# Optimization experiments

Hardware: AMD Instinct MI355X
Metric: run time of the kernel (lower is better)

The kernel has to match this reference:

```python
import jax, jax.numpy as jnp
import numpy as np

D_MODEL = 1024
D_STATE = 16
D_CONV = 4
EXPAND = 2
D_INNER = D_MODEL * EXPAND
B_SZ = 2
SEQ = 4096


def setup_inputs() -> dict:
    key = jax.random.key(0)
    ks = jax.random.split(key, 11)
    rn = lambda i, shape, scale=1.0: jax.random.normal(ks[i], shape, jnp.float32) * scale
    return {
        "x": rn(0, (B_SZ, SEQ, D_MODEL)),
        "W_in": rn(1, (D_MODEL, D_INNER), D_MODEL ** -0.5),
        "b_in": rn(2, (D_INNER,), 0.01),
        "conv_w": rn(3, (D_INNER, 1, D_CONV), 0.1),   # torch depthwise layout [out_ch, in_ch/groups=1, k]
        "conv_b": rn(4, (D_INNER,), 0.01),
        # A scaled so tanh(A) is contractive -> stable recurrence over 4096 steps
        "A": rn(5, (D_STATE, D_STATE), 0.1),
        "Bp": rn(6, (D_STATE,)),   # B parameter [d_state, 1] flattened
        "Cp": rn(7, (D_STATE,)),   # C parameter [1, d_state] flattened
        "Dp": rn(8, (1,)),
        "W_out": rn(9, (D_INNER, D_MODEL), D_INNER ** -0.5),
        "b_out": rn(10, (D_MODEL,), 0.01),
    }


def reference(x, W_in, b_in, conv_w, conv_b, A, Bp, Cp, Dp, W_out, b_out):
    Bsz, S, _ = x.shape
    d_inner = W_in.shape[1]
    # input projection
    u = x @ W_in + b_in                              # [B, S, d_inner]
    # causal depthwise conv (torch pads k-1 both sides then slices [:S])
    u = u.transpose(0, 2, 1)                         # [B, d_inner, S]
    u = jax.lax.conv_general_dilated(
        u, conv_w, window_strides=(1,), padding=[(D_CONV - 1, 0)],
        dimension_numbers=("NCH", "OIH", "NCH"),
        feature_group_count=d_inner) + conv_b[None, :, None]
    u = u.transpose(0, 2, 1)                         # [B, S, d_inner]
    # per-channel scalar SSM shared across channels: h_t = tanh(A) h_{t-1} + B u_t; y_t = C h_t + D u_t
    At = jnp.tanh(A)                                 # [ds, ds]
    def step(h, u_t):                                # h: [B, d_inner, ds], u_t: [B, d_inner]
        h = jnp.einsum("ij,bdj->bdi", At, h) + u_t[..., None] * Bp
        y = jnp.einsum("j,bdj->bd", Cp, h) + Dp[0] * u_t
        return h, y
    h0 = jnp.zeros((Bsz, d_inner, Bp.shape[0]), x.dtype)
    _, ys = jax.lax.scan(step, h0, u.transpose(1, 0, 2))  # ys: [S, B, d_inner]
    y = jax.nn.silu(ys.transpose(1, 0, 2))           # [B, S, d_inner]
    return y @ W_out + b_out                         # [B, S, d_model]
```

## Files before the change

kernel.cpp:

```cpp
#include <hip/hip_runtime.h>

typedef unsigned short u16;
typedef float  f32x4  __attribute__((ext_vector_type(4)));
typedef __bf16 bf16x8 __attribute__((ext_vector_type(8)));
typedef u16    u16x2  __attribute__((ext_vector_type(2)));
typedef u16    u16x4  __attribute__((ext_vector_type(4)));

#define D_MODEL 1024
#define D_INNER 2048
#define B_SZ    2
#define SEQ     4096
#define MROWS   (B_SZ * SEQ)
#define LTAPS   64
#define VROW    136

__device__ __forceinline__ u16 f2bf(float f) {
    return __builtin_bit_cast(u16, (__bf16)f);
}
__device__ __forceinline__ float bf2f(u16 h) {
    unsigned u = ((unsigned)h) << 16;
    return __builtin_bit_cast(float, u);
}

typedef __attribute__((address_space(1))) void gv_t;
typedef __attribute__((address_space(3))) void lv_t;
__device__ __forceinline__ void glds16(const u16* g, u16* l) {
    __builtin_amdgcn_global_load_lds((gv_t*)g, (lv_t*)l, 16, 0, 0);
}
#define WAIT_VM0   0x0F70
#define WAIT_LGKM0 0xC07F

__device__ __forceinline__ void transpose_tile(
    const float* __restrict__ in, u16* __restrict__ out,
    int R, int C, int c0, int r0, int tid, float (*tile)[33])
{
    const int tx = tid & 31, ty = tid >> 5;
    for (int k = 0; k < 32; k += 8)
        tile[ty + k][tx] = in[(size_t)(r0 + ty + k) * C + c0 + tx];
    __syncthreads();
    for (int k = 0; k < 32; k += 8)
        out[(size_t)(c0 + ty + k) * R + r0 + tx] = f2bf(tile[tx][ty + k]);
}

__global__ __launch_bounds__(256) void prep_kernel(
    const float* __restrict__ x, u16* __restrict__ xb,
    const float* __restrict__ Win, u16* __restrict__ WinT,
    const float* __restrict__ Wout, u16* __restrict__ WoutT,
    const float* __restrict__ A, const float* __restrict__ Bp,
    const float* __restrict__ Cp, const float* __restrict__ Dp,
    u16* __restrict__ Amat64)
{
    __shared__ float tile[32][33];
    __shared__ float fs[LTAPS];
    const int bx = blockIdx.x, tid = threadIdx.x;
    if (bx < 8192) {
        size_t i = ((size_t)bx * 256 + tid) * 4;
        f32x4 v = *(const f32x4*)(x + i);
        u16x4 o;
        o.x = f2bf(v.x); o.y = f2bf(v.y); o.z = f2bf(v.z); o.w = f2bf(v.w);
        *(u16x4*)(xb + i) = o;
    } else if (bx < 10240) {
        const int flat = bx - 8192;
        transpose_tile(Win, WinT, 1024, 2048,
                       (flat & 63) * 32, (flat >> 6) * 32, tid, tile);
    } else if (bx < 12288) {
        const int flat = bx - 10240;
        transpose_tile(Wout, WoutT, 2048, 1024,
                       (flat & 31) * 32, (flat >> 5) * 32, tid, tile);
    } else {
        if (tid < 64) {
            const int i = tid & 15;
            float Atr[16];
            for (int j = 0; j < 16; j++) Atr[j] = tanhf(A[i * 16 + j]);
            float p = Bp[i];
            const float c  = Cp[i];
            const float d0 = Dp[0];
            for (int t = 0; t < LTAPS; t++) {
                float fv = c * p;
                fv += __shfl_xor(fv, 1); fv += __shfl_xor(fv, 2);
                fv += __shfl_xor(fv, 4); fv += __shfl_xor(fv, 8);
                if (tid == 0) fs[t] = fv + (t == 0 ? d0 : 0.f);
                float n0 = 0.f, n1 = 0.f, n2 = 0.f, n3 = 0.f;
                #pragma unroll
                for (int j = 0; j < 4; j++) {
                    n0 = fmaf(Atr[j],      __shfl(p, j),      n0);
                    n1 = fmaf(Atr[j + 4],  __shfl(p, j + 4),  n1);
                    n2 = fmaf(Atr[j + 8],  __shfl(p, j + 8),  n2);
                    n3 = fmaf(Atr[j + 12], __shfl(p, j + 12), n3);
                }
                p = (n0 + n1) + (n2 + n3);
            }
        }
        __syncthreads();
        for (int idx = tid; idx < 64 * 128; idx += 256) {
            const int i = idx >> 7, j = idx & 127;
            const int tau = 64 + i - j;
            float v = (tau >= 0 && tau < LTAPS) ? fs[tau] : 0.f;
            Amat64[idx] = f2bf(v);
        }
    }
}

template <int MODE>
__global__ __launch_bounds__(256) void gemm_bt_kernel(
    const u16* __restrict__ A, const u16* __restrict__ BT,
    void* __restrict__ Cout, const float* __restrict__ bias,
    int M, int N, int K)
{
    __shared__ u16 As[128 * 32];
    __shared__ u16 Bs[128 * 32];
    const int tid = threadIdx.x, lane = tid & 63, wid = tid >> 6;
    const int nTiles = gridDim.x;
    const int bid = blockIdx.x + nTiles * blockIdx.y;
    const int xcd = bid & 7;
    const int loc = bid >> 3;
    const int mt  = xcd * (gridDim.y >> 3) + (loc & 7);
    const int nt  = loc >> 3;
    const int m0 = mt * 128, n0 = nt * 128;
    const int sr = wid * 32 + (lane >> 2);
    const int sc = (lane & 3) * 8;
    const u16* ga = A  + (size_t)(m0 + sr) * K + sc;
    const u16* gb = BT + (size_t)(n0 + sr) * K + sc;
    u16* la = As + wid * 1024;
    u16* lb = Bs + wid * 1024;
    const int wm = (wid & 1) * 64, wn = (wid >> 1) * 64;
    const int fr = lane & 15, fq = lane >> 4;
    f32x4 acc[4][4] = {};
    glds16(ga, la);
    glds16(ga + (size_t)16 * K, la + 512);
    glds16(gb, lb);
    glds16(gb + (size_t)16 * K, lb + 512);
    const int iters = K >> 5;
    for (int it = 0; it < iters; ++it) {
        __builtin_amdgcn_s_waitcnt(WAIT_VM0);
        __builtin_amdgcn_s_barrier();
        bf16x8 af[4], bfr[4];
        #pragma unroll
        for (int i = 0; i < 4; i++)
            af[i]  = *(const bf16x8*)(As + (wm + i * 16 + fr) * 32 + fq * 8);
        #pragma unroll
        for (int i = 0; i < 4; i++)
            bfr[i] = *(const bf16x8*)(Bs + (wn + i * 16 + fr) * 32 + fq * 8);
        asm volatile("" ::: "memory");
        __builtin_amdgcn_s_waitcnt(WAIT_LGKM0);
        __builtin_amdgcn_s_barrier();
        if (it + 1 < iters) {
            const int k0 = (it + 1) << 5;
            glds16(ga + k0, la);
            glds16(ga + k0 + (size_t)16 * K, la + 512);
            glds16(gb + k0, lb);
            glds16(gb + k0 + (size_t)16 * K, lb + 512);
        }
        #pragma unroll
        for (int mi = 0; mi < 4; mi++)
            #pragma unroll
            for (int ni = 0; ni < 4; ni++)
                acc[mi][ni] = __builtin_amdgcn_mfma_f32_16x16x32_bf16(
                    bfr[ni], af[mi], acc[mi][ni], 0, 0, 0);
    }
    for (int ni = 0; ni < 4; ni++) {
        const int colb = n0 + wn + ni * 16 + fq * 4;
        const f32x4 bv = *(const f32x4*)(bias + colb);
        for (int mi = 0; mi < 4; mi++) {
            const int row = m0 + wm + mi * 16 + fr;
            f32x4 v = acc[mi][ni];
            v.x += bv.x; v.y += bv.y; v.z += bv.z; v.w += bv.w;
            if constexpr (MODE == 0) {
                u16x4 o;
                o.x = f2bf(v.x); o.y = f2bf(v.y); o.z = f2bf(v.z); o.w = f2bf(v.w);
                *(u16x4*)((u16*)Cout + (size_t)row * N + colb) = o;
            } else {
                *(f32x4*)((float*)Cout + (size_t)row * N + colb) = v;
            }
        }
    }
}

__global__ __launch_bounds__(256) void conv_fir_mfma_kernel(
    const u16* __restrict__ u, const float* __restrict__ cw,
    const float* __restrict__ cb, const u16* __restrict__ Amat64,
    u16* __restrict__ Y)
{
    __shared__ u16 VT[128 * VROW];
    const int tid = threadIdx.x;
    const int c0 = blockIdx.x * 128, t0 = blockIdx.y * 64, b = blockIdx.z;
    {
        const int tx = tid & 63, ty = tid >> 6;
        const int cg = c0 + tx * 2;
        const f32x4 wA = *(const f32x4*)(cw + cg * 4);
        const f32x4 wB = *(const f32x4*)(cw + cg * 4 + 4);
        const float cb0 = cb[cg], cb1 = cb[cg + 1];
        const u16* ucol = u + (size_t)b * SEQ * D_INNER + cg;
        const int s0 = t0 - 64 + ty * 32;
        u16* vr0 = VT + (tx * 2)     * VROW + ty * 32;
        u16* vr1 = VT + (tx * 2 + 1) * VROW + ty * 32;
        if (t0 == 0 && ty < 2) {
            const u16x4 z = {0, 0, 0, 0};
            #pragma unroll
            for (int j = 0; j < 8; j++) {
                *(u16x4*)(vr0 + j * 4) = z;
                *(u16x4*)(vr1 + j * 4) = z;
            }
        } else {
            float am3 = 0.f, am2 = 0.f, am1 = 0.f;
            float bm3 = 0.f, bm2 = 0.f, bm1 = 0.f;
            if (s0 > 0) {
                u16x2 d3 = *(const u16x2*)(ucol + (size_t)(s0 - 3) * D_INNER);
                u16x2 d2 = *(const u16x2*)(ucol + (size_t)(s0 - 2) * D_INNER);
                u16x2 d1 = *(const u16x2*)(ucol + (size_t)(s0 - 1) * D_INNER);
                am3 = bf2f(d3.x); bm3 = bf2f(d3.y);
                am2 = bf2f(d2.x); bm2 = bf2f(d2.y);
                am1 = bf2f(d1.x); bm1 = bf2f(d1.y);
            }
            #pragma unroll 2
            for (int j = 0; j < 8; j++) {
                const u16* p = ucol + (size_t)(s0 + j * 4) * D_INNER;
                u16x2 r0 = *(const u16x2*)(p);
                u16x2 r1 = *(const u16x2*)(p + (size_t)D_INNER);
                u16x2 r2 = *(const u16x2*)(p + (size_t)2 * D_INNER);
                u16x2 r3 = *(const u16x2*)(p + (size_t)3 * D_INNER);
                float a0 = bf2f(r0.x), b0 = bf2f(r0.y);
                float a1 = bf2f(r1.x), b1 = bf2f(r1.y);
                float a2 = bf2f(r2.x), b2 = bf2f(r2.y);
                float a3 = bf2f(r3.x), b3 = bf2f(r3.y);
                u16x4 oa, ob;
                oa.x = f2bf(cb0 + wA.x * am3 + wA.y * am2 + wA.z * am1 + wA.w * a0);
                oa.y = f2bf(cb0 + wA.x * am2 + wA.y * am1 + wA.z * a0  + wA.w * a1);
                oa.z = f2bf(cb0 + wA.x * am1 + wA.y * a0  + wA.z * a1  + wA.w * a2);
                oa.w = f2bf(cb0 + wA.x * a0  + wA.y * a1  + wA.z * a2  + wA.w * a3);
                ob.x = f2bf(cb1 + wB.x * bm3 + wB.y * bm2 + wB.z * bm1 + wB.w * b0);
                ob.y = f2bf(cb1 + wB.x * bm2 + wB.y * bm1 + wB.z * b0  + wB.w * b1);
                ob.z = f2bf(cb1 + wB.x * bm1 + wB.y * b0  + wB.z * b1  + wB.w * b2);
                ob.w = f2bf(cb1 + wB.x * b0  + wB.y * b1  + wB.z * b2  + wB.w * b3);
                *(u16x4*)(vr0 + j * 4) = oa;
                *(u16x4*)(vr1 + j * 4) = ob;
                am3 = a1; am2 = a2; am1 = a3;
                bm3 = b1; bm2 = b2; bm1 = b3;
            }
        }
    }
    __syncthreads();
    const int lane = tid & 63, wid = tid >> 6;
    const int wm = (wid & 1) * 32, wn = (wid >> 1) * 64;
    const int fr = lane & 15, fq = lane >> 4;
    f32x4 acc[2][4] = {};
    #pragma unroll
    for (int kq = 0; kq < 4; kq++) {
        const int k0 = kq * 32;
        bf16x8 af[2], bfr[4];
        #pragma unroll
        for (int mi = 0; mi < 2; mi++)
            af[mi] = *(const bf16x8*)(Amat64 + (wm + mi * 16 + fr) * 128 + k0 + fq * 8);
        #pragma unroll
        for (int ni = 0; ni < 4; ni++)
            bfr[ni] = *(const bf16x8*)(VT + (wn + ni * 16 + fr) * VROW + k0 + fq * 8);
        #pragma unroll
        for (int mi = 0; mi < 2; mi++)
            #pragma unroll
            for (int ni = 0; ni < 4; ni++)
                acc[mi][ni] = __builtin_amdgcn_mfma_f32_16x16x32_bf16(
                    bfr[ni], af[mi], acc[mi][ni], 0, 0, 0);
    }
    #pragma unroll
    for (int ni = 0; ni < 4; ni++) {
        const int cbase = c0 + wn + ni * 16 + fq * 4;
        #pragma unroll
        for (int mi = 0; mi < 2; mi++) {
            const int trow = t0 + wm + mi * 16 + fr;
            f32x4 v = acc[mi][ni];
            u16x4 o;
            o.x = f2bf(v.x / (1.f + __expf(-v.x)));
            o.y = f2bf(v.y / (1.f + __expf(-v.y)));
            o.z = f2bf(v.z / (1.f + __expf(-v.z)));
            o.w = f2bf(v.w / (1.f + __expf(-v.w)));
            *(u16x4*)(Y + ((size_t)(b * SEQ + trow)) * D_INNER + cbase) = o;
        }
    }
}

extern "C" void kernel_launch(void* const* d_in, const int* in_sizes, int n_in,
                              void* d_out, int out_size, void* d_ws, size_t ws_size,
                              hipStream_t stream)
{
    const float* x    = (const float*)d_in[0];
    const float* Win  = (const float*)d_in[1];
    const float* bin  = (const float*)d_in[2];
    const float* cw   = (const float*)d_in[3];
    const float* cb   = (const float*)d_in[4];
    const float* A    = (const float*)d_in[5];
    const float* Bp   = (const float*)d_in[6];
    const float* Cp   = (const float*)d_in[7];
    const float* Dp   = (const float*)d_in[8];
    const float* Wout = (const float*)d_in[9];
    const float* bout = (const float*)d_in[10];
    float* out = (float*)d_out;

    char* ws = (char*)d_ws;
    u16* xb     = (u16*)(ws);
    u16* WinT   = (u16*)(ws + 16777216);
    u16* WoutT  = (u16*)(ws + 20971520);
    u16* u      = (u16*)(ws + 25165824);
    u16* Y      = (u16*)(ws + 58720256);
    u16* Amat64 = (u16*)(ws + 92274688);

    prep_kernel<<<12289, 256, 0, stream>>>(x, xb, Win, WinT, Wout, WoutT,
                                           A, Bp, Cp, Dp, Amat64);
    gemm_bt_kernel<0><<<dim3(16, 64), 256, 0, stream>>>(xb, WinT, u, bin,
                                                        MROWS, D_INNER, D_MODEL);
    conv_fir_mfma_kernel<<<dim3(16, 64, 2), 256, 0, stream>>>(u, cw, cb, Amat64, Y);
    gemm_bt_kernel<1><<<dim3(8, 64), 256, 0, stream>>>(Y, WoutT, out, bout,
                                                       MROWS, D_MODEL, D_INNER);
}
```

Measured before the change: 241.1 us.

## Double-buffer GEMM LDS tiles and enlarge FIR conv time tile to 128

```diff
diff --git a/kernel.cpp b/kernel.cpp
--- a/kernel.cpp
+++ b/kernel.cpp
@@ -12,7 +12,8 @@
 #define SEQ     4096
 #define MROWS   (B_SZ * SEQ)
 #define LTAPS   64
-#define VROW    136
+#define KFIR    192
+#define CVROW   200
 
 __device__ __forceinline__ u16 f2bf(float f) {
     return __builtin_bit_cast(u16, (__bf16)f);
@@ -28,7 +29,9 @@
     __builtin_amdgcn_global_load_lds((gv_t*)g, (lv_t*)l, 16, 0, 0);
 }
 #define WAIT_VM0   0x0F70
+#define WAIT_VM4   0x0F74
 #define WAIT_LGKM0 0xC07F
+#define SCHED_FENCE() asm volatile("" ::: "memory")
 
 __device__ __forceinline__ void transpose_tile(
     const float* __restrict__ in, u16* __restrict__ out,
@@ -48,7 +51,7 @@
     const float* __restrict__ Wout, u16* __restrict__ WoutT,
     const float* __restrict__ A, const float* __restrict__ Bp,
     const float* __restrict__ Cp, const float* __restrict__ Dp,
-    u16* __restrict__ Amat64)
+    u16* __restrict__ Amat192)
 {
     __shared__ float tile[32][33];
     __shared__ float fs[LTAPS];
@@ -92,11 +95,11 @@
             }
         }
         __syncthreads();
-        for (int idx = tid; idx < 64 * 128; idx += 256) {
-            const int i = idx >> 7, j = idx & 127;
+        for (int idx = tid; idx < 128 * KFIR; idx += 256) {
+            const int i = idx / KFIR, j = idx % KFIR;
             const int tau = 64 + i - j;
             float v = (tau >= 0 && tau < LTAPS) ? fs[tau] : 0.f;
-            Amat64[idx] = f2bf(v);
+            Amat192[idx] = f2bf(v);
         }
     }
 }
@@ -107,8 +110,8 @@
     void* __restrict__ Cout, const float* __restrict__ bias,
     int M, int N, int K)
 {
-    __shared__ u16 As[128 * 32];
-    __shared__ u16 Bs[128 * 32];
+    __shared__ u16 As[2][128 * 32];
+    __shared__ u16 Bs[2][128 * 32];
     const int tid = threadIdx.x, lane = tid & 63, wid = tid >> 6;
     const int nTiles = gridDim.x;
     const int bid = blockIdx.x + nTiles * blockIdx.y;
@@ -121,34 +124,44 @@
     const int sc = (lane & 3) * 8;
     const u16* ga = A  + (size_t)(m0 + sr) * K + sc;
     const u16* gb = BT + (size_t)(n0 + sr) * K + sc;
-    u16* la = As + wid * 1024;
-    u16* lb = Bs + wid * 1024;
+    const int lo = wid * 1024;
     const int wm = (wid & 1) * 64, wn = (wid >> 1) * 64;
     const int fr = lane & 15, fq = lane >> 4;
     f32x4 acc[4][4] = {};
-    glds16(ga, la);
-    glds16(ga + (size_t)16 * K, la + 512);
-    glds16(gb, lb);
-    glds16(gb + (size_t)16 * K, lb + 512);
+    glds16(ga,                    As[0] + lo);
+    glds16(ga + (size_t)16 * K,   As[0] + lo + 512);
+    glds16(gb,                    Bs[0] + lo);
+    glds16(gb + (size_t)16 * K,   Bs[0] + lo + 512);
+    glds16(ga + 32,               As[1] + lo);
+    glds16(ga + 32 + (size_t)16 * K, As[1] + lo + 512);
+    glds16(gb + 32,               Bs[1] + lo);
+    glds16(gb + 32 + (size_t)16 * K, Bs[1] + lo + 512);
     const int iters = K >> 5;
     for (int it = 0; it < iters; ++it) {
-        __builtin_amdgcn_s_waitcnt(WAIT_VM0);
+        if (it + 1 < iters) __builtin_amdgcn_s_waitcnt(WAIT_VM4);
+        else                __builtin_amdgcn_s_waitcnt(WAIT_VM0);
         __builtin_amdgcn_s_barrier();
+        SCHED_FENCE();
+        const u16* Ab = As[it & 1];
+        const u16* Bb = Bs[it & 1];
         bf16x8 af[4], bfr[4];
         #pragma unroll
         for (int i = 0; i < 4; i++)
-            af[i]  = *(const bf16x8*)(As + (wm + i * 16 + fr) * 32 + fq * 8);
+            af[i]  = *(const bf16x8*)(Ab + (wm + i * 16 + fr) * 32 + fq * 8);
         #pragma unroll
         for (int i = 0; i < 4; i++)
-            bfr[i] = *(const bf16x8*)(Bs + (wn + i * 16 + fr) * 32 + fq * 8);
-        asm volatile("" ::: "memory");
+            bfr[i] = *(const bf16x8*)(Bb + (wn + i * 16 + fr) * 32 + fq * 8);
+        SCHED_FENCE();
         __builtin_amdgcn_s_waitcnt(WAIT_LGKM0);
         __builtin_amdgcn_s_barrier();
-        if (it + 1 < iters) {
-            const int k0 = (it + 1) << 5;
-            glds16(ga + k0, la);
+        SCHED_FENCE();
+        if (it + 2 < iters) {
+            const int k0 = (it + 2) << 5;
+            u16* la = As[it & 1] + lo;
+            u16* lb = Bs[it & 1] + lo;
+            glds16(ga + k0,                  la);
             glds16(ga + k0 + (size_t)16 * K, la + 512);
-            glds16(gb + k0, lb);
+            glds16(gb + k0,                  lb);
             glds16(gb + k0 + (size_t)16 * K, lb + 512);
         }
         #pragma unroll
@@ -178,12 +191,12 @@
 
 __global__ __launch_bounds__(256) void conv_fir_mfma_kernel(
     const u16* __restrict__ u, const float* __restrict__ cw,
-    const float* __restrict__ cb, const u16* __restrict__ Amat64,
+    const float* __restrict__ cb, const u16* __restrict__ Amat192,
     u16* __restrict__ Y)
 {
-    __shared__ u16 VT[128 * VROW];
+    __shared__ u16 VT[128 * CVROW];
     const int tid = threadIdx.x;
-    const int c0 = blockIdx.x * 128, t0 = blockIdx.y * 64, b = blockIdx.z;
+    const int c0 = blockIdx.x * 128, t0 = blockIdx.y * 128, b = blockIdx.z;
     {
         const int tx = tid & 63, ty = tid >> 6;
         const int cg = c0 + tx * 2;
@@ -191,30 +204,28 @@
         const f32x4 wB = *(const f32x4*)(cw + cg * 4 + 4);
         const float cb0 = cb[cg], cb1 = cb[cg + 1];
         const u16* ucol = u + (size_t)b * SEQ * D_INNER + cg;
-        const int s0 = t0 - 64 + ty * 32;
-        u16* vr0 = VT + (tx * 2)     * VROW + ty * 32;
-        u16* vr1 = VT + (tx * 2 + 1) * VROW + ty * 32;
-        if (t0 == 0 && ty < 2) {
-            const u16x4 z = {0, 0, 0, 0};
-            #pragma unroll
-            for (int j = 0; j < 8; j++) {
+        const int sbase = t0 - 64 + ty * 48;
+        u16* vr0 = VT + (tx * 2)     * CVROW + ty * 48;
+        u16* vr1 = VT + (tx * 2 + 1) * CVROW + ty * 48;
+        float am3 = 0.f, am2 = 0.f, am1 = 0.f;
+        float bm3 = 0.f, bm2 = 0.f, bm1 = 0.f;
+        if (sbase > 0) {
+            u16x2 d3 = *(const u16x2*)(ucol + (size_t)(sbase - 3) * D_INNER);
+            u16x2 d2 = *(const u16x2*)(ucol + (size_t)(sbase - 2) * D_INNER);
+            u16x2 d1 = *(const u16x2*)(ucol + (size_t)(sbase - 1) * D_INNER);
+            am3 = bf2f(d3.x); bm3 = bf2f(d3.y);
+            am2 = bf2f(d2.x); bm2 = bf2f(d2.y);
+            am1 = bf2f(d1.x); bm1 = bf2f(d1.y);
+        }
+        #pragma unroll 4
+        for (int j = 0; j < 12; j++) {
+            const int sq = sbase + j * 4;
+            if (sq < 0) {
+                const u16x4 z = {0, 0, 0, 0};
                 *(u16x4*)(vr0 + j * 4) = z;
                 *(u16x4*)(vr1 + j * 4) = z;
-            }
-        } else {
-            float am3 = 0.f, am2 = 0.f, am1 = 0.f;
-            float bm3 = 0.f, bm2 = 0.f, bm1 = 0.f;
-            if (s0 > 0) {
-                u16x2 d3 = *(const u16x2*)(ucol + (size_t)(s0 - 3) * D_INNER);
-                u16x2 d2 = *(const u16x2*)(ucol + (size_t)(s0 - 2) * D_INNER);
-                u16x2 d1 = *(const u16x2*)(ucol + (size_t)(s0 - 1) * D_INNER);
-                am3 = bf2f(d3.x); bm3 = bf2f(d3.y);
-                am2 = bf2f(d2.x); bm2 = bf2f(d2.y);
-                am1 = bf2f(d1.x); bm1 = bf2f(d1.y);
-            }
-            #pragma unroll 2
-            for (int j = 0; j < 8; j++) {
-                const u16* p = ucol + (size_t)(s0 + j * 4) * D_INNER;
+            } else {
+                const u16* p = ucol + (size_t)sq * D_INNER;
                 u16x2 r0 = *(const u16x2*)(p);
                 u16x2 r1 = *(const u16x2*)(p + (size_t)D_INNER);
                 u16x2 r2 = *(const u16x2*)(p + (size_t)2 * D_INNER);
@@ -241,21 +252,21 @@
     }
     __syncthreads();
     const int lane = tid & 63, wid = tid >> 6;
-    const int wm = (wid & 1) * 32, wn = (wid >> 1) * 64;
+    const int wm = (wid & 1) * 64, wn = (wid >> 1) * 64;
     const int fr = lane & 15, fq = lane >> 4;
-    f32x4 acc[2][4] = {};
+    f32x4 acc[4][4] = {};
     #pragma unroll
-    for (int kq = 0; kq < 4; kq++) {
+    for (int kq = 0; kq < 6; kq++) {
         const int k0 = kq * 32;
-        bf16x8 af[2], bfr[4];
-        #pragma unroll
-        for (int mi = 0; mi < 2; mi++)
-            af[mi] = *(const bf16x8*)(Amat64 + (wm + mi * 16 + fr) * 128 + k0 + fq * 8);
+        bf16x8 af[4], bfr[4];
+        #pragma unroll
+        for (int mi = 0; mi < 4; mi++)
+            af[mi] = *(const bf16x8*)(Amat192 + (wm + mi * 16 + fr) * KFIR + k0 + fq * 8);
         #pragma unroll
         for (int ni = 0; ni < 4; ni++)
-            bfr[ni] = *(const bf16x8*)(VT + (wn + ni * 16 + fr) * VROW + k0 + fq * 8);
-        #pragma unroll
-        for (int mi = 0; mi < 2; mi++)
+            bfr[ni] = *(const bf16x8*)(VT + (wn + ni * 16 + fr) * CVROW + k0 + fq * 8);
+        #pragma unroll
+        for (int mi = 0; mi < 4; mi++)
             #pragma unroll
             for (int ni = 0; ni < 4; ni++)
                 acc[mi][ni] = __builtin_amdgcn_mfma_f32_16x16x32_bf16(
@@ -265,7 +276,7 @@
     for (int ni = 0; ni < 4; ni++) {
         const int cbase = c0 + wn + ni * 16 + fq * 4;
         #pragma unroll
-        for (int mi = 0; mi < 2; mi++) {
+        for (int mi = 0; mi < 4; mi++) {
             const int trow = t0 + wm + mi * 16 + fr;
             f32x4 v = acc[mi][ni];
             u16x4 o;
@@ -296,18 +307,18 @@
     float* out = (float*)d_out;
 
     char* ws = (char*)d_ws;
-    u16* xb     = (u16*)(ws);
-    u16* WinT   = (u16*)(ws + 16777216);
-    u16* WoutT  = (u16*)(ws + 20971520);
-    u16* u      = (u16*)(ws + 25165824);
-    u16* Y      = (u16*)(ws + 58720256);
-    u16* Amat64 = (u16*)(ws + 92274688);
+    u16* xb      = (u16*)(ws);
+    u16* WinT    = (u16*)(ws + 16777216);
+    u16* WoutT   = (u16*)(ws + 20971520);
+    u16* u       = (u16*)(ws + 25165824);
+    u16* Y       = (u16*)(ws + 58720256);
+    u16* Amat192 = (u16*)(ws + 92274688);
 
     prep_kernel<<<12289, 256, 0, stream>>>(x, xb, Win, WinT, Wout, WoutT,
-                                           A, Bp, Cp, Dp, Amat64);
+                                           A, Bp, Cp, Dp, Amat192);
     gemm_bt_kernel<0><<<dim3(16, 64), 256, 0, stream>>>(xb, WinT, u, bin,
                                                         MROWS, D_INNER, D_MODEL);
-    conv_fir_mfma_kernel<<<dim3(16, 64, 2), 256, 0, stream>>>(u, cw, cb, Amat64, Y);
+    conv_fir_mfma_kernel<<<dim3(16, 32, 2), 256, 0, stream>>>(u, cw, cb, Amat192, Y);
     gemm_bt_kernel<1><<<dim3(8, 64), 256, 0, stream>>>(Y, WoutT, out, bout,
                                                        MROWS, D_MODEL, D_INNER);
 }
```

After: 257.5 us. 1.07x slower.

## Load B fragments directly from global into registers and widen K tile

Applied to the files above, without the earlier changes.

```diff
diff --git a/kernel.cpp b/kernel.cpp
--- a/kernel.cpp
+++ b/kernel.cpp
@@ -28,7 +28,10 @@
     __builtin_amdgcn_global_load_lds((gv_t*)g, (lv_t*)l, 16, 0, 0);
 }
 #define WAIT_VM0   0x0F70
+#define WAIT_VM4   0x0F74
+#define WAIT_VM8   0x0F78
 #define WAIT_LGKM0 0xC07F
+#define SCHED_FENCE() asm volatile("" ::: "memory")
 
 __device__ __forceinline__ void transpose_tile(
     const float* __restrict__ in, u16* __restrict__ out,
@@ -107,8 +110,7 @@
     void* __restrict__ Cout, const float* __restrict__ bias,
     int M, int N, int K)
 {
-    __shared__ u16 As[128 * 32];
-    __shared__ u16 Bs[128 * 32];
+    __shared__ u16 As[128 * 64];
     const int tid = threadIdx.x, lane = tid & 63, wid = tid >> 6;
     const int nTiles = gridDim.x;
     const int bid = blockIdx.x + nTiles * blockIdx.y;
@@ -117,46 +119,59 @@
     const int mt  = xcd * (gridDim.y >> 3) + (loc & 7);
     const int nt  = loc >> 3;
     const int m0 = mt * 128, n0 = nt * 128;
-    const int sr = wid * 32 + (lane >> 2);
-    const int sc = (lane & 3) * 8;
-    const u16* ga = A  + (size_t)(m0 + sr) * K + sc;
-    const u16* gb = BT + (size_t)(n0 + sr) * K + sc;
-    u16* la = As + wid * 1024;
-    u16* lb = Bs + wid * 1024;
+    const int sr = wid * 32 + (lane >> 3);
+    const int sc = (lane & 7) * 8;
+    const u16* ga = A + (size_t)(m0 + sr) * K + sc;
+    u16* la = As + wid * 2048;
     const int wm = (wid & 1) * 64, wn = (wid >> 1) * 64;
     const int fr = lane & 15, fq = lane >> 4;
+    const u16* gB = BT + (size_t)(n0 + wn + fr) * K + fq * 8;
     f32x4 acc[4][4] = {};
-    glds16(ga, la);
-    glds16(ga + (size_t)16 * K, la + 512);
-    glds16(gb, lb);
-    glds16(gb + (size_t)16 * K, lb + 512);
-    const int iters = K >> 5;
+    #pragma unroll
+    for (int r = 0; r < 32; r += 8)
+        glds16(ga + (size_t)r * K, la + r * 64);
+    const int iters = K >> 6;
     for (int it = 0; it < iters; ++it) {
-        __builtin_amdgcn_s_waitcnt(WAIT_VM0);
+        const int k0 = it << 6;
+        SCHED_FENCE();
+        bf16x8 bfr[4][2];
+        #pragma unroll
+        for (int ni = 0; ni < 4; ni++)
+            #pragma unroll
+            for (int kk = 0; kk < 2; kk++)
+                bfr[ni][kk] = *(const bf16x8*)(gB + (size_t)(ni * 16) * K + k0 + kk * 32);
+        SCHED_FENCE();
+        __builtin_amdgcn_s_waitcnt(WAIT_VM8);
         __builtin_amdgcn_s_barrier();
-        bf16x8 af[4], bfr[4];
+        SCHED_FENCE();
+        bf16x8 af[4][2];
         #pragma unroll
         for (int i = 0; i < 4; i++)
-            af[i]  = *(const bf16x8*)(As + (wm + i * 16 + fr) * 32 + fq * 8);
-        #pragma unroll
-        for (int i = 0; i < 4; i++)
-            bfr[i] = *(const bf16x8*)(Bs + (wn + i * 16 + fr) * 32 + fq * 8);
-        asm volatile("" ::: "memory");
+            #pragma unroll
+            for (int kk = 0; kk < 2; kk++)
+                af[i][kk] = *(const bf16x8*)(As + (wm + i * 16 + fr) * 64 + kk * 32 + fq * 8);
+        SCHED_FENCE();
         __builtin_amdgcn_s_waitcnt(WAIT_LGKM0);
         __builtin_amdgcn_s_barrier();
+        SCHED_FENCE();
         if (it + 1 < iters) {
-            const int k0 = (it + 1) << 5;
-            glds16(ga + k0, la);
-            glds16(ga + k0 + (size_t)16 * K, la + 512);
-            glds16(gb + k0, lb);
-            glds16(gb + k0 + (size_t)16 * K, lb + 512);
-        }
-        #pragma unroll
-        for (int mi = 0; mi < 4; mi++)
-            #pragma unroll
-            for (int ni = 0; ni < 4; ni++)
-                acc[mi][ni] = __builtin_amdgcn_mfma_f32_16x16x32_bf16(
-                    bfr[ni], af[mi], acc[mi][ni], 0, 0, 0);
+            const int kn = (it + 1) << 6;
+            #pragma unroll
+            for (int r = 0; r < 32; r += 8)
+                glds16(ga + kn + (size_t)r * K, la + r * 64);
+            __builtin_amdgcn_s_waitcnt(WAIT_VM4);
+        } else {
+            __builtin_amdgcn_s_waitcnt(WAIT_VM0);
+        }
+        SCHED_FENCE();
+        #pragma unroll
+        for (int kk = 0; kk < 2; kk++)
+            #pragma unroll
+            for (int mi = 0; mi < 4; mi++)
+                #pragma unroll
+                for (int ni = 0; ni < 4; ni++)
+                    acc[mi][ni] = __builtin_amdgcn_mfma_f32_16x16x32_bf16(
+                        bfr[ni][kk], af[mi][kk], acc[mi][ni], 0, 0, 0);
     }
     for (int ni = 0; ni < 4; ni++) {
         const int colb = n0 + wn + ni * 16 + fq * 4;
```

Result: slower. 298.5 us (+23.8%).
